# Kernel tuning notes

Measured on AMD Instinct MI355X. Metric: run time of the kernel, lower is better.

## Reference

```python
import jax, jax.numpy as jnp
import numpy as np

H = 200  # hidden size
D = 1    # input size
T = 8192 # sequence length


def setup_inputs() -> dict:
    key = jax.random.key(0)
    ks = jax.random.split(key, 11)
    s = 1.0 / np.sqrt(H)  # torch LSTM init scale
    u = lambda k, shape: jax.random.uniform(k, shape, jnp.float32, -s, s)
    return {
        "input_seq": jax.random.normal(ks[0], (T, D), jnp.float32),
        "W_ih0": u(ks[1], (4 * H, D)),
        "W_hh0": u(ks[2], (4 * H, H)),
        "b_ih0": u(ks[3], (4 * H,)),
        "b_hh0": u(ks[4], (4 * H,)),
        "W_ih1": u(ks[5], (4 * H, H)),
        "W_hh1": u(ks[6], (4 * H, H)),
        "b_ih1": u(ks[7], (4 * H,)),
        "b_hh1": u(ks[8], (4 * H,)),
        "W_out": u(ks[9], (D, H)),
        "b_out": u(ks[10], (D,)),
    }


def _cell(pre, h, c, Whh):
    # pre: [4H] = x @ W_ih.T + b_ih + b_hh already folded in
    g = pre + h @ Whh.T
    i, f, gg, o = jnp.split(g, 4)
    i = jax.nn.sigmoid(i)
    f = jax.nn.sigmoid(f)
    gg = jnp.tanh(gg)
    o = jax.nn.sigmoid(o)
    c = f * c + i * gg
    h = o * jnp.tanh(c)
    return h, c


def reference(input_seq, W_ih0, W_hh0, b_ih0, b_hh0,
              W_ih1, W_hh1, b_ih1, b_hh1, W_out, b_out):
    x = input_seq.reshape(input_seq.shape[0], -1)  # [T, D]
    # precompute layer-0 input projections for all timesteps (one big GEMM)
    pre0 = x @ W_ih0.T + (b_ih0 + b_hh0)           # [T, 4H]
    b1 = b_ih1 + b_hh1

    def step(carry, p0):
        h0, c0, h1, c1 = carry
        h0, c0 = _cell(p0, h0, c0, W_hh0)
        # eval mode: dropout(0.1) between layers is identity
        h1, c1 = _cell(h0 @ W_ih1.T + b1, h1, c1, W_hh1)
        return (h0, c0, h1, c1), None

    z = jnp.zeros((H,), x.dtype)
    (h0, c0, h1, c1), _ = jax.lax.scan(step, (z, z, z, z), pre0)
    # predictions[-1]: linear head on last top-layer hidden state -> [D]
    return h1 @ W_out.T + b_out
```

## Files before the change

### kernel.cpp

```cpp
#include <hip/hip_runtime.h>

#define TT 8192
#define HH 200
#define RD 1024
#define RDM 1023
#define BPWIN 900

typedef unsigned long long u64;
typedef unsigned int u32;
typedef _Float16 f16;
typedef _Float16 f16x2 __attribute__((ext_vector_type(2)));

__device__ __forceinline__ float sigmoidf_(float x){ return 1.0f/(1.0f+__expf(-x)); }
__device__ __forceinline__ float tanhf_(float x){
    float e = __expf(2.0f*fabsf(x));
    float r = 1.0f - 2.0f/(e + 1.0f);
    return copysignf(r, x);
}
__device__ __forceinline__ u64 pcku(u32 tag, u32 v){ return ((u64)tag<<32) | v; }
__device__ __forceinline__ u64 pckf(u32 tag, float v){ return pcku(tag, __float_as_uint(v)); }
__device__ __forceinline__ u64 ald(const u64* p){
    return __hip_atomic_load((u64*)p, __ATOMIC_RELAXED, __HIP_MEMORY_SCOPE_AGENT);
}
__device__ __forceinline__ void ast(u64* p, u64 v){
    __hip_atomic_store(p, v, __ATOMIC_RELAXED, __HIP_MEMORY_SCOPE_AGENT);
}
__device__ __forceinline__ u32 pkh(float a, float b){
    f16x2 v = { (f16)a, (f16)b };
    return __builtin_bit_cast(u32, v);
}
__device__ __forceinline__ float unpk(u32 u, int hi){
    f16x2 v = __builtin_bit_cast(f16x2, u);
    return (float)v[hi];
}
__device__ __forceinline__ float dot2(u32 a, u32 b, float c){
#if __has_builtin(__builtin_amdgcn_fdot2)
    return __builtin_amdgcn_fdot2(__builtin_bit_cast(f16x2, a),
                                  __builtin_bit_cast(f16x2, b), c, false);
#else
    f16x2 av = __builtin_bit_cast(f16x2, a), bv = __builtin_bit_cast(f16x2, b);
    return c + (float)av[0]*(float)bv[0] + (float)av[1]*(float)bv[1];
#endif
}
__device__ __forceinline__ u32 poll1u(const u64* p, u32 tag){
    u64 v; do { v = ald(p); } while ((u32)(v >> 32) != tag);
    return (u32)v;
}

__device__ __forceinline__ void poll100(const u64* base, u32 tag, int l,
                                        u32* o0, u32* o1){
    const bool g1 = (l + 64 < 100);
    u64 v0, v1 = 0;
    for(;;){
        v0 = ald(base + l);
        if (g1) v1 = ald(base + l + 64);
        if ((u32)(v0>>32)==tag && (!g1 || (u32)(v1>>32)==tag)) break;
    }
    *o0 = (u32)v0;
    *o1 = (u32)v1;
}

__global__ __launch_bounds__(512)
__attribute__((amdgpu_waves_per_eu(2, 4)))
void lstm_pipe(const float* __restrict__ x,
               const float* __restrict__ Wih0, const float* __restrict__ Whh0,
               const float* __restrict__ bih0, const float* __restrict__ bhh0,
               const float* __restrict__ Wih1, const float* __restrict__ Whh1,
               const float* __restrict__ bih1, const float* __restrict__ bhh1,
               const float* __restrict__ Wout, const float* __restrict__ bout,
               u64* __restrict__ hp0,
               u64* __restrict__ p1r,
               u64* __restrict__ h1x,
               u32* __restrict__ prog,
               float* __restrict__ out)
{
    const int bid = blockIdx.x;
    const int tid = threadIdx.x;

    __shared__ __align__(16) u32 wl[3 * 400 * 4];
    __shared__ float xs[TT];
    __shared__ __align__(16) u32 hp_lds[2][100];
    __shared__ u32 hpbuf[2][100];
    __shared__ float s_pre[400];
    __shared__ float s_in[2][400];
    __shared__ float h32[100];
    __shared__ float pad_f[6656];

    if (x == nullptr) pad_f[0] = 1.f;

    int role = -1, L = 0, hf = 0, q = 0;
    if      (bid == 0)  { role = 0; L = 0; hf = 0; }
    else if (bid == 8)  { role = 0; L = 0; hf = 1; }
    else if (bid == 1)  { role = 0; L = 1; hf = 0; }
    else if (bid == 9)  { role = 0; L = 1; hf = 1; }
    else if (bid == 2)  { role = 1; q = 0; }
    else if (bid == 10) { role = 1; q = 1; }
    else if (bid == 3)  { role = 1; q = 2; }
    else if (bid == 11) { role = 1; q = 3; }
    if (role < 0) return;

    if (role == 1) {
        const int rl = tid >> 1, kh = tid & 1;
        const bool act = (tid < 400);
        u32 wp[50]; float bs = 0.f; int row = 0;
        if (act) {
            row = q * 200 + rl;
            const float* wr = Wih1 + (size_t)row * HH + kh * 100;
            #pragma unroll
            for (int i = 0; i < 50; ++i) wp[i] = pkh(wr[2*i], wr[2*i+1]);
            #pragma unroll
            for (int i = 0; i < 50; ++i) asm volatile("" : "+v"(wp[i]));
            if (kh == 0) bs = bih1[row] + bhh1[row];
        } else if (tid >= 448) {
            u32 o0, o1;
            poll100(hp0, 1u, tid - 448, &o0, &o1);
            hpbuf[0][tid - 448] = o0;
            if (tid - 448 + 64 < 100) hpbuf[0][tid - 448 + 64] = o1;
        }
        u32 prog_c = 0;
        __syncthreads();
        for (int t = 0; t < TT; ++t) {
            if (act) {
                const u32* hb = hpbuf[t & 1] + kh * 50;
                float a0 = 0.f, a1 = 0.f;
                #pragma unroll
                for (int i = 0; i < 50; i += 2) a0 = dot2(wp[i], hb[i], a0);
                #pragma unroll
                for (int i = 1; i < 50; i += 2) a1 = dot2(wp[i], hb[i], a1);
                float s = a0 + a1;
                s += __shfl_xor(s, 1);
                if (kh == 0)
                    ast(&p1r[(size_t)(t & RDM) * 800 + q * 200 + rl],
                        pckf((u32)(t + 1), s + bs));
            } else if (tid >= 448) {
                if (t + 1 < TT) {
                    u32 o0, o1;
                    poll100(&hp0[(size_t)(t + 1) * 100], (u32)(t + 2),
                            tid - 448, &o0, &o1);
                    hpbuf[(t + 1) & 1][tid - 448] = o0;
                    if (tid - 448 + 64 < 100) hpbuf[(t + 1) & 1][tid - 448 + 64] = o1;
                }
            } else if (tid == 440) {
                while ((int)(t + 1) - (int)prog_c >= BPWIN) {
                    __builtin_amdgcn_s_sleep(8);
                    prog_c = __hip_atomic_load(prog, __ATOMIC_RELAXED,
                                               __HIP_MEMORY_SCOPE_AGENT);
                }
            }
            __syncthreads();
        }
        return;
    }

    const int nb = hf * 100;
    const int pb = (1 - hf) * 100;
    const float* Whh = L ? Whh1 : Whh0;
    const bool act = (tid < 400);

    for (int idx = tid; idx < 400 * 12; idx += 512) {
        const int rl = idx / 12, pp = idx % 12;
        const int row = (rl / 100) * 200 + nb + (rl % 100);
        wl[(((pp >> 2) * 400) + rl) * 4 + (pp & 3)] =
            pkh(Whh[(size_t)row * HH + 2*pp], Whh[(size_t)row * HH + 2*pp + 1]);
    }
    u32 w[88]; float wih = 0.f, bs = 0.f;
    if (act) {
        const int row = (tid / 100) * 200 + nb + (tid % 100);
        const float* wr = Whh + (size_t)row * HH + 24;
        #pragma unroll
        for (int i = 0; i < 88; ++i) w[i] = pkh(wr[2*i], wr[2*i + 1]);
        #pragma unroll
        for (int i = 0; i < 88; ++i) asm volatile("" : "+v"(w[i]));
        if (L == 0) {
            bs = bih0[row] + bhh0[row];
            wih = Wih0[row];
            asm volatile("" : "+v"(bs));
            asm volatile("" : "+v"(wih));
        }
    }
    if (L == 0) for (int i = tid; i < TT; i += 512) xs[i] = x[i];
    if (tid < 100) { hp_lds[0][tid] = 0u; hp_lds[1][tid] = 0u; h32[tid] = 0.f; }

    u32 ov[7];
    if (L == 1 && tid >= 448) {
        const int l = tid - 448;
        int sl[7]; bool g[7];
        #pragma unroll
        for (int r = 0; r < 7; ++r) {
            const int m = l + 64 * r;
            g[r] = (m < 400);
            sl[r] = g[r] ? (m / 100) * 200 + nb + (m % 100) : 0;
        }
        u64 v[7];
        for(;;){
            #pragma unroll
            for (int r = 0; r < 7; ++r) if (g[r]) v[r] = ald(&p1r[sl[r]]);
            bool ok = true;
            #pragma unroll
            for (int r = 0; r < 7; ++r) if (g[r] && (u32)(v[r]>>32) != 1u) ok = false;
            if (ok) break;
        }
        #pragma unroll
        for (int r = 0; r < 7; ++r)
            if (g[r]) s_in[0][l + 64 * r] = __uint_as_float((u32)v[r]);
    }
    float c = 0.f;
    __syncthreads();

    for (int t = 0; t < TT; ++t) {
        const int p = t & 1;
        if (act) {
            const uint4* hp4 = (const uint4*)hp_lds[p];
            float a0=0.f, a1=0.f, a2=0.f, a3=0.f;
            #pragma unroll
            for (int g2 = 0; g2 < 3; ++g2) {
                const uint4 hu = hp4[g2];
                const uint4 wu = *(const uint4*)&wl[((g2 * 400) + tid) << 2];
                a0 = dot2(wu.x, hu.x, a0);
                a1 = dot2(wu.y, hu.y, a1);
                a2 = dot2(wu.z, hu.z, a2);
                a3 = dot2(wu.w, hu.w, a3);
            }
            #pragma unroll
            for (int g2 = 3; g2 < 25; ++g2) {
                const uint4 hu = hp4[g2];
                const int i = (g2 - 3) * 4;
                a0 = dot2(w[i],     hu.x, a0);
                a1 = dot2(w[i + 1], hu.y, a1);
                a2 = dot2(w[i + 2], hu.z, a2);
                a3 = dot2(w[i + 3], hu.w, a3);
            }
            const float acc = (a0 + a1) + (a2 + a3);
            s_pre[tid] = acc + ((L == 0) ? xs[t] * wih + bs : s_in[p][tid]);
        } else if (L == 1 && tid >= 448 && t + 1 < TT) {
            const int l = tid - 448;
            u64 v[7];
            const u64* slot = &p1r[(size_t)((t + 1) & RDM) * 800];
            const u32 tg = (u32)(t + 2);
            for(;;){
                #pragma unroll
                for (int r = 0; r < 7; ++r) {
                    const int m = l + 64 * r;
                    if (m < 400) v[r] = ald(slot + (m/100)*200 + nb + (m%100));
                }
                bool ok = true;
                #pragma unroll
                for (int r = 0; r < 7; ++r) {
                    const int m = l + 64 * r;
                    if (m < 400 && (u32)(v[r]>>32) != tg) ok = false;
                }
                if (ok) break;
            }
            #pragma unroll
            for (int r = 0; r < 7; ++r) ov[r] = (u32)v[r];
        }
        __syncthreads();
        if (tid < 100) {
            const int n = tid;
            const float ig = sigmoidf_(s_pre[n]);
            const float fg = sigmoidf_(s_pre[100 + n]);
            const float gg = tanhf_  (s_pre[200 + n]);
            const float og = sigmoidf_(s_pre[300 + n]);
            c = fg * c + ig * gg;
            const float h = og * tanhf_(c);
            h32[n] = h;
            const float hq = __shfl_xor(h, 1);
            if (!(n & 1)) {
                const u32 pk = pkh(h, hq);
                hp_lds[p ^ 1][(nb >> 1) + (n >> 1)] = pk;
                if (L == 0)
                    ast(&hp0[(size_t)t * 100 + (nb >> 1) + (n >> 1)],
                        pcku((u32)(t + 1), pk));
                else
                    ast(&h1x[(size_t)(t & 63) * 100 + (nb >> 1) + (n >> 1)],
                        pcku((u32)(t + 1), pk));
            }
        } else if (tid >= 448) {
            const int l = tid - 448;
            if (L == 1 && t + 1 < TT) {
                #pragma unroll
                for (int r = 0; r < 7; ++r) {
                    const int m = l + 64 * r;
                    if (m < 400) s_in[p ^ 1][m] = __uint_as_float(ov[r]);
                }
            }
            if (l < 50) {
                const u64* src = (L == 0)
                    ? &hp0[(size_t)t * 100 + (pb >> 1) + l]
                    : &h1x[(size_t)(t & 63) * 100 + (pb >> 1) + l];
                hp_lds[p ^ 1][(pb >> 1) + l] = poll1u(src, (u32)(t + 1));
            }
        } else if (L == 1 && hf == 0 && tid == 400 && (t & 63) == 63) {
            __hip_atomic_store(prog, (u32)(t + 1), __ATOMIC_RELAXED,
                               __HIP_MEMORY_SCOPE_AGENT);
        }
        __syncthreads();
    }

    if (L == 1 && hf == 0 && tid < 64) {
        const int fin = ((TT - 1) & 1) ^ 1;
        float s2 = 0.f;
        for (int k = tid; k < HH; k += 64) {
            float hv;
            if (k < 100) hv = h32[k];
            else         hv = unpk(hp_lds[fin][50 + ((k - 100) >> 1)], (k - 100) & 1);
            s2 += hv * Wout[k];
        }
        #pragma unroll
        for (int off = 32; off > 0; off >>= 1) s2 += __shfl_down(s2, off);
        if (tid == 0) out[0] = s2 + bout[0];
    }
}

extern "C" void kernel_launch(void* const* d_in, const int* in_sizes, int n_in,
                              void* d_out, int out_size, void* d_ws, size_t ws_size,
                              hipStream_t stream) {
    const float* x    = (const float*)d_in[0];
    const float* Wih0 = (const float*)d_in[1];
    const float* Whh0 = (const float*)d_in[2];
    const float* bih0 = (const float*)d_in[3];
    const float* bhh0 = (const float*)d_in[4];
    const float* Wih1 = (const float*)d_in[5];
    const float* Whh1 = (const float*)d_in[6];
    const float* bih1 = (const float*)d_in[7];
    const float* bhh1 = (const float*)d_in[8];
    const float* Wout = (const float*)d_in[9];
    const float* bout = (const float*)d_in[10];
    float* out = (float*)d_out;

    char* ws = (char*)d_ws;
    u64* hp0  = (u64*)ws;
    u64* p1r  = (u64*)(ws + 6553600);
    u64* h1x  = (u64*)(ws + 13107200);
    u32* prog = (u32*)(ws + 13158400);

    hipMemsetAsync(ws, 0, 13158464, stream);

    hipLaunchKernelGGL(lstm_pipe, dim3(16), dim3(512), 0, stream,
        x, Wih0, Whh0, bih0, bhh0, Wih1, Whh1, bih1, bhh1, Wout, bout,
        hp0, p1r, h1x, prog, out);
}
```

Baseline: 14.70 ms.

## Use MFMA 16x16x32 for recurrent matvec in LSTM recurrence blocks

Replaces the per-thread fp16 dot2 recurrent matvec (weights split between registers and LDS) with wave-level MFMA 16x16x32 f16 ops. Each of 8 waves holds weight tiles in registers for 48 rows, and the 16 leftover rows are handled by dot2 plus shuffle reductions. Input-projection and bias addition move into the gate-activation threads, and the layer-1 input polling moves to a separate phase, which may shorten the critical path. It only uses one column of the MFMA output and removes the LDS padding array, which can change occupancy.

```diff
diff --git a/kernel.cpp b/kernel.cpp
--- a/kernel.cpp
+++ b/kernel.cpp
@@ -10,6 +10,8 @@
 typedef unsigned int u32;
 typedef _Float16 f16;
 typedef _Float16 f16x2 __attribute__((ext_vector_type(2)));
+typedef _Float16 half8 __attribute__((ext_vector_type(8)));
+typedef float f32x4 __attribute__((ext_vector_type(4)));
 
 __device__ __forceinline__ float sigmoidf_(float x){ return 1.0f/(1.0f+__expf(-x)); }
 __device__ __forceinline__ float tanhf_(float x){
@@ -46,7 +48,6 @@
     u64 v; do { v = ald(p); } while ((u32)(v >> 32) != tag);
     return (u32)v;
 }
-
 __device__ __forceinline__ void poll100(const u64* base, u32 tag, int l,
                                         u32* o0, u32* o1){
     const bool g1 = (l + 64 < 100);
@@ -77,16 +78,13 @@
     const int bid = blockIdx.x;
     const int tid = threadIdx.x;
 
-    __shared__ __align__(16) u32 wl[3 * 400 * 4];
     __shared__ float xs[TT];
-    __shared__ __align__(16) u32 hp_lds[2][100];
+    __shared__ __align__(16) u32 hp_lds[2][112];
     __shared__ u32 hpbuf[2][100];
     __shared__ float s_pre[400];
     __shared__ float s_in[2][400];
+    __shared__ float wihL[400], bsL[400];
     __shared__ float h32[100];
-    __shared__ float pad_f[6656];
-
-    if (x == nullptr) pad_f[0] = 1.f;
 
     int role = -1, L = 0, hf = 0, q = 0;
     if      (bid == 0)  { role = 0; L = 0; hf = 0; }
@@ -155,112 +153,128 @@
     const int nb = hf * 100;
     const int pb = (1 - hf) * 100;
     const float* Whh = L ? Whh1 : Whh0;
-    const bool act = (tid < 400);
-
-    for (int idx = tid; idx < 400 * 12; idx += 512) {
-        const int rl = idx / 12, pp = idx % 12;
-        const int row = (rl / 100) * 200 + nb + (rl % 100);
-        wl[(((pp >> 2) * 400) + rl) * 4 + (pp & 3)] =
-            pkh(Whh[(size_t)row * HH + 2*pp], Whh[(size_t)row * HH + 2*pp + 1]);
-    }
-    u32 w[88]; float wih = 0.f, bs = 0.f;
-    if (act) {
-        const int row = (tid / 100) * 200 + nb + (tid % 100);
-        const float* wr = Whh + (size_t)row * HH + 24;
+
+    const int wv = tid >> 6, ln = tid & 63;
+    const int lrow16 = ln & 15, lkgrp = ln >> 4;
+
+    uint4 au[3][7];
+    #pragma unroll
+    for (int tt2 = 0; tt2 < 3; ++tt2) {
+        const int rl = 16 * (wv * 3 + tt2) + lrow16;
+        const int g  = (rl / 100) * 200 + nb + (rl % 100);
+        const float* wr = Whh + (size_t)g * HH;
         #pragma unroll
-        for (int i = 0; i < 88; ++i) w[i] = pkh(wr[2*i], wr[2*i + 1]);
+        for (int kt = 0; kt < 7; ++kt) {
+            const int kb = kt * 32 + lkgrp * 8;
+            float w8[8];
+            #pragma unroll
+            for (int e = 0; e < 8; ++e) w8[e] = (kb + e < HH) ? wr[kb + e] : 0.f;
+            au[tt2][kt] = make_uint4(pkh(w8[0],w8[1]), pkh(w8[2],w8[3]),
+                                     pkh(w8[4],w8[5]), pkh(w8[6],w8[7]));
+            asm volatile("" : "+v"(au[tt2][kt].x), "+v"(au[tt2][kt].y),
+                              "+v"(au[tt2][kt].z), "+v"(au[tt2][kt].w));
+        }
+    }
+    u32 wr7[7]; int remrow = 0;
+    if (wv < 4) {
+        remrow = 384 + wv * 4 + lkgrp;
+        const int g = (remrow / 100) * 200 + nb + (remrow % 100);
+        const float* wr = Whh + (size_t)g * HH;
         #pragma unroll
-        for (int i = 0; i < 88; ++i) asm volatile("" : "+v"(w[i]));
-        if (L == 0) {
-            bs = bih0[row] + bhh0[row];
-            wih = Wih0[row];
-            asm volatile("" : "+v"(bs));
-            asm volatile("" : "+v"(wih));
-        }
-    }
-    if (L == 0) for (int i = tid; i < TT; i += 512) xs[i] = x[i];
-    if (tid < 100) { hp_lds[0][tid] = 0u; hp_lds[1][tid] = 0u; h32[tid] = 0.f; }
-
-    u32 ov[7];
-    if (L == 1 && tid >= 448) {
-        const int l = tid - 448;
-        int sl[7]; bool g[7];
-        #pragma unroll
-        for (int r = 0; r < 7; ++r) {
-            const int m = l + 64 * r;
-            g[r] = (m < 400);
-            sl[r] = g[r] ? (m / 100) * 200 + nb + (m % 100) : 0;
-        }
+        for (int j = 0; j < 7; ++j) {
+            const int k = 14 * lrow16 + 2 * j;
+            wr7[j] = pkh(k < HH ? wr[k] : 0.f, k + 1 < HH ? wr[k+1] : 0.f);
+            asm volatile("" : "+v"(wr7[j]));
+        }
+    }
+    if (L == 0) {
+        for (int i = tid; i < TT; i += 512) xs[i] = x[i];
+        if (tid < 400) {
+            const int g = (tid / 100) * 200 + nb + (tid % 100);
+            wihL[tid] = Wih0[g];
+            bsL[tid]  = bih0[g] + bhh0[g];
+        }
+    }
+    if (tid < 112) { hp_lds[0][tid] = 0u; hp_lds[1][tid] = 0u; }
+    if (tid < 100) h32[tid] = 0.f;
+
+    if (L == 1 && wv == 6) {
         u64 v[7];
         for(;;){
             #pragma unroll
-            for (int r = 0; r < 7; ++r) if (g[r]) v[r] = ald(&p1r[sl[r]]);
+            for (int r2 = 0; r2 < 7; ++r2) {
+                const int m = ln + 64 * r2;
+                if (m < 400) v[r2] = ald(&p1r[(m/100)*200 + nb + (m%100)]);
+            }
             bool ok = true;
             #pragma unroll
-            for (int r = 0; r < 7; ++r) if (g[r] && (u32)(v[r]>>32) != 1u) ok = false;
+            for (int r2 = 0; r2 < 7; ++r2) {
+                const int m = ln + 64 * r2;
+                if (m < 400 && (u32)(v[r2]>>32) != 1u) ok = false;
+            }
             if (ok) break;
         }
         #pragma unroll
-        for (int r = 0; r < 7; ++r)
-            if (g[r]) s_in[0][l + 64 * r] = __uint_as_float((u32)v[r]);
+        for (int r2 = 0; r2 < 7; ++r2) {
+            const int m = ln + 64 * r2;
+            if (m < 400) s_in[0][m] = __uint_as_float((u32)v[r2]);
+        }
     }
     float c = 0.f;
     __syncthreads();
 
     for (int t = 0; t < TT; ++t) {
         const int p = t & 1;
-        if (act) {
+        {
+            f32x4 d0 = {0.f,0.f,0.f,0.f}, d1 = {0.f,0.f,0.f,0.f},
+                  d2 = {0.f,0.f,0.f,0.f};
             const uint4* hp4 = (const uint4*)hp_lds[p];
-            float a0=0.f, a1=0.f, a2=0.f, a3=0.f;
-            #pragma unroll
-            for (int g2 = 0; g2 < 3; ++g2) {
-                const uint4 hu = hp4[g2];
-                const uint4 wu = *(const uint4*)&wl[((g2 * 400) + tid) << 2];
-                a0 = dot2(wu.x, hu.x, a0);
-                a1 = dot2(wu.y, hu.y, a1);
-                a2 = dot2(wu.z, hu.z, a2);
-                a3 = dot2(wu.w, hu.w, a3);
-            }
-            #pragma unroll
-            for (int g2 = 3; g2 < 25; ++g2) {
-                const uint4 hu = hp4[g2];
-                const int i = (g2 - 3) * 4;
-                a0 = dot2(w[i],     hu.x, a0);
-                a1 = dot2(w[i + 1], hu.y, a1);
-                a2 = dot2(w[i + 2], hu.z, a2);
-                a3 = dot2(w[i + 3], hu.w, a3);
-            }
-            const float acc = (a0 + a1) + (a2 + a3);
-            s_pre[tid] = acc + ((L == 0) ? xs[t] * wih + bs : s_in[p][tid]);
-        } else if (L == 1 && tid >= 448 && t + 1 < TT) {
-            const int l = tid - 448;
-            u64 v[7];
-            const u64* slot = &p1r[(size_t)((t + 1) & RDM) * 800];
-            const u32 tg = (u32)(t + 2);
-            for(;;){
-                #pragma unroll
-                for (int r = 0; r < 7; ++r) {
-                    const int m = l + 64 * r;
-                    if (m < 400) v[r] = ald(slot + (m/100)*200 + nb + (m%100));
-                }
-                bool ok = true;
-                #pragma unroll
-                for (int r = 0; r < 7; ++r) {
-                    const int m = l + 64 * r;
-                    if (m < 400 && (u32)(v[r]>>32) != tg) ok = false;
-                }
-                if (ok) break;
-            }
-            #pragma unroll
-            for (int r = 0; r < 7; ++r) ov[r] = (u32)v[r];
+            #pragma unroll
+            for (int kt = 0; kt < 7; ++kt) {
+                const half8 b = __builtin_bit_cast(half8, hp4[kt * 4 + lkgrp]);
+                d0 = __builtin_amdgcn_mfma_f32_16x16x32_f16(
+                         __builtin_bit_cast(half8, au[0][kt]), b, d0, 0, 0, 0);
+                d1 = __builtin_amdgcn_mfma_f32_16x16x32_f16(
+                         __builtin_bit_cast(half8, au[1][kt]), b, d1, 0, 0, 0);
+                d2 = __builtin_amdgcn_mfma_f32_16x16x32_f16(
+                         __builtin_bit_cast(half8, au[2][kt]), b, d2, 0, 0, 0);
+            }
+            if (lrow16 == 0) {
+                const int rb = lkgrp * 4;
+                #pragma unroll
+                for (int r2 = 0; r2 < 4; ++r2) {
+                    s_pre[16*(wv*3+0) + rb + r2] = d0[r2];
+                    s_pre[16*(wv*3+1) + rb + r2] = d1[r2];
+                    s_pre[16*(wv*3+2) + rb + r2] = d2[r2];
+                }
+            }
+            if (wv < 4) {
+                float s = 0.f;
+                #pragma unroll
+                for (int j = 0; j < 7; ++j)
+                    s = dot2(wr7[j], hp_lds[p][7*lrow16 + j], s);
+                s += __shfl_xor(s, 1); s += __shfl_xor(s, 2);
+                s += __shfl_xor(s, 4); s += __shfl_xor(s, 8);
+                if (lrow16 == 0) s_pre[remrow] = s;
+            }
         }
         __syncthreads();
         if (tid < 100) {
             const int n = tid;
-            const float ig = sigmoidf_(s_pre[n]);
-            const float fg = sigmoidf_(s_pre[100 + n]);
-            const float gg = tanhf_  (s_pre[200 + n]);
-            const float og = sigmoidf_(s_pre[300 + n]);
+            float g0 = s_pre[n],       g1 = s_pre[100 + n],
+                  g2 = s_pre[200 + n], g3 = s_pre[300 + n];
+            if (L == 0) {
+                const float xv = xs[t];
+                g0 += xv * wihL[n]       + bsL[n];
+                g1 += xv * wihL[100 + n] + bsL[100 + n];
+                g2 += xv * wihL[200 + n] + bsL[200 + n];
+                g3 += xv * wihL[300 + n] + bsL[300 + n];
+            } else {
+                g0 += s_in[p][n];       g1 += s_in[p][100 + n];
+                g2 += s_in[p][200 + n]; g3 += s_in[p][300 + n];
+            }
+            const float ig = sigmoidf_(g0), fg = sigmoidf_(g1);
+            const float gg = tanhf_(g2),    og = sigmoidf_(g3);
             c = fg * c + ig * gg;
             const float h = og * tanhf_(c);
             h32[n] = h;
@@ -275,22 +289,39 @@
                     ast(&h1x[(size_t)(t & 63) * 100 + (nb >> 1) + (n >> 1)],
                         pcku((u32)(t + 1), pk));
             }
-        } else if (tid >= 448) {
-            const int l = tid - 448;
-            if (L == 1 && t + 1 < TT) {
-                #pragma unroll
-                for (int r = 0; r < 7; ++r) {
-                    const int m = l + 64 * r;
-                    if (m < 400) s_in[p ^ 1][m] = __uint_as_float(ov[r]);
-                }
-            }
-            if (l < 50) {
+        } else if (wv == 7) {
+            if (ln < 50) {
                 const u64* src = (L == 0)
-                    ? &hp0[(size_t)t * 100 + (pb >> 1) + l]
-                    : &h1x[(size_t)(t & 63) * 100 + (pb >> 1) + l];
-                hp_lds[p ^ 1][(pb >> 1) + l] = poll1u(src, (u32)(t + 1));
-            }
-        } else if (L == 1 && hf == 0 && tid == 400 && (t & 63) == 63) {
+                    ? &hp0[(size_t)t * 100 + (pb >> 1) + ln]
+                    : &h1x[(size_t)(t & 63) * 100 + (pb >> 1) + ln];
+                hp_lds[p ^ 1][(pb >> 1) + ln] = poll1u(src, (u32)(t + 1));
+            }
+        } else if (L == 1 && wv == 6) {
+            if (t + 1 < TT) {
+                const u64* slot = &p1r[(size_t)((t + 1) & RDM) * 800];
+                const u32 tg = (u32)(t + 2);
+                u64 v[7];
+                for(;;){
+                    #pragma unroll
+                    for (int r2 = 0; r2 < 7; ++r2) {
+                        const int m = ln + 64 * r2;
+                        if (m < 400) v[r2] = ald(slot + (m/100)*200 + nb + (m%100));
+                    }
+                    bool ok = true;
+                    #pragma unroll
+                    for (int r2 = 0; r2 < 7; ++r2) {
+                        const int m = ln + 64 * r2;
+                        if (m < 400 && (u32)(v[r2]>>32) != tg) ok = false;
+                    }
+                    if (ok) break;
+                }
+                #pragma unroll
+                for (int r2 = 0; r2 < 7; ++r2) {
+                    const int m = ln + 64 * r2;
+                    if (m < 400) s_in[p ^ 1][m] = __uint_as_float((u32)v[r2]);
+                }
+            }
+        } else if (L == 1 && hf == 0 && tid == 100 && (t & 63) == 63) {
             __hip_atomic_store(prog, (u32)(t + 1), __ATOMIC_RELAXED,
                                __HIP_MEMORY_SCOPE_AGENT);
         }
```

Result: faster. 14.16 ms (-3.7%).
